# Kernel tuning notes

Hardware: AMD Instinct MI355X
Metric: run time of the kernel (lower is better)

Reference implementation:

```python
import jax, jax.numpy as jnp
import numpy as np


def setup_inputs() -> dict:
    key = jax.random.key(0)
    k1, k2 = jax.random.split(key)
    B, N, D = 32, 8192, 64
    x = jax.random.normal(k1, (B, N, D), dtype=jnp.float32)
    y = jax.random.normal(k2, (B, D, N), dtype=jnp.float32)
    return {"x": x, "y": y}


def reference(x, y):
    # Original: full cdist [B,N,N], mean over batch, take diagonal.
    # Only matched pairs (i,i) survive, so compute them directly —
    # mathematically identical output and gradients.
    y_t = jnp.transpose(y, (0, 2, 1))          # [B, N, D]
    diff = x - y_t                             # [B, N, D]
    pair_dist = jnp.sqrt(jnp.sum(diff * diff, axis=-1))  # [B, N]
    dist_diag = jnp.mean(pair_dist, axis=0)    # [N] == diag(mean_b cdist)
    dist_diag = dist_diag.at[1:3].multiply(1.5)
    loss = jnp.mean(dist_diag)
    return loss
```

## Files before the change

kernel.cpp:

```cpp
#include <hip/hip_runtime.h>


constexpr int B = 32;
constexpr int N = 8192;
constexpr int D = 64;

__global__ __launch_bounds__(256) void euclid_loss_kernel(
    const float* __restrict__ x,
    const float* __restrict__ y,
    float* __restrict__ out)
{
    const int tid = threadIdx.x;
    const int n   = blockIdx.x * 256 + tid;
    const int b   = blockIdx.y;

    const float* xrow = x + ((size_t)b * N + n) * D;
    const float* ycol = y + (size_t)b * D * N + n;

    float acc = 0.0f;
#pragma unroll
    for (int d = 0; d < D; d += 4) {
        const float4 xv = *reinterpret_cast<const float4*>(xrow + d);
        const float y0 = ycol[(size_t)(d + 0) * N];
        const float y1 = ycol[(size_t)(d + 1) * N];
        const float y2 = ycol[(size_t)(d + 2) * N];
        const float y3 = ycol[(size_t)(d + 3) * N];
        const float d0 = xv.x - y0;
        const float d1 = xv.y - y1;
        const float d2 = xv.z - y2;
        const float d3 = xv.w - y3;
        acc += d0 * d0 + d1 * d1 + d2 * d2 + d3 * d3;
    }

    const float w = (n == 1 || n == 2) ? 1.5f : 1.0f;
    float v = w * sqrtf(acc);

#pragma unroll
    for (int off = 32; off > 0; off >>= 1) v += __shfl_down(v, off, 64);

    __shared__ float wsum[4];
    if ((tid & 63) == 0) wsum[tid >> 6] = v;
    __syncthreads();

    if (tid == 0) {
        const float s = (wsum[0] + wsum[1] + wsum[2] + wsum[3]) *
                        (1.0f / (float)(B * N));
        atomicAdd(out, s);
    }
}

extern "C" void kernel_launch(void* const* d_in, const int* in_sizes, int n_in,
                              void* d_out, int out_size, void* d_ws, size_t ws_size,
                              hipStream_t stream) {
    const float* x = (const float*)d_in[0];
    const float* y = (const float*)d_in[1];
    float* out = (float*)d_out;

    hipMemsetAsync(out, 0, sizeof(float), stream);

    dim3 grid(N / 256, B);
    euclid_loss_kernel<<<grid, 256, 0, stream>>>(x, y, out);
}
```

Before: 150.7 us.

## Split each pair's reduction across four threads to improve coalescing and parallelism

Each matched pair is now handled by four threads, each covering sixteen of the feature dimensions, with a shuffle-based reduction combining the partials. All loads are issued up front into registers. The grid grows fourfold, aiming for better x coalescing and more memory-level parallelism. In exchange, y loads are split into smaller contiguous segments and extra shuffles are needed.

```diff
diff --git a/kernel.cpp b/kernel.cpp
--- a/kernel.cpp
+++ b/kernel.cpp
@@ -4,39 +4,53 @@
 constexpr int B = 32;
 constexpr int N = 8192;
 constexpr int D = 64;
+constexpr int TPP = 4;
+constexpr int DC  = D / TPP;
+constexpr int PAIRS_PER_BLOCK = 256 / TPP;
 
 __global__ __launch_bounds__(256) void euclid_loss_kernel(
     const float* __restrict__ x,
     const float* __restrict__ y,
     float* __restrict__ out)
 {
-    const int tid = threadIdx.x;
-    const int n   = blockIdx.x * 256 + tid;
-    const int b   = blockIdx.y;
+    const int tid   = threadIdx.x;
+    const int pair  = tid >> 2;
+    const int chunk = tid & 3;
+    const int n     = blockIdx.x * PAIRS_PER_BLOCK + pair;
+    const int b     = blockIdx.y;
 
-    const float* xrow = x + ((size_t)b * N + n) * D;
-    const float* ycol = y + (size_t)b * D * N + n;
+    const float* xp = x + ((size_t)b * N + n) * D + chunk * DC;
+    const float* yp = y + (size_t)b * D * N + (size_t)(chunk * DC) * N + n;
+
+    float4 xv[4];
+#pragma unroll
+    for (int j = 0; j < 4; ++j)
+        xv[j] = *reinterpret_cast<const float4*>(xp + 4 * j);
+
+    float yv[DC];
+#pragma unroll
+    for (int d = 0; d < DC; ++d)
+        yv[d] = yp[(size_t)d * N];
 
     float acc = 0.0f;
 #pragma unroll
-    for (int d = 0; d < D; d += 4) {
-        const float4 xv = *reinterpret_cast<const float4*>(xrow + d);
-        const float y0 = ycol[(size_t)(d + 0) * N];
-        const float y1 = ycol[(size_t)(d + 1) * N];
-        const float y2 = ycol[(size_t)(d + 2) * N];
-        const float y3 = ycol[(size_t)(d + 3) * N];
-        const float d0 = xv.x - y0;
-        const float d1 = xv.y - y1;
-        const float d2 = xv.z - y2;
-        const float d3 = xv.w - y3;
+    for (int j = 0; j < 4; ++j) {
+        const float d0 = xv[j].x - yv[4 * j + 0];
+        const float d1 = xv[j].y - yv[4 * j + 1];
+        const float d2 = xv[j].z - yv[4 * j + 2];
+        const float d3 = xv[j].w - yv[4 * j + 3];
         acc += d0 * d0 + d1 * d1 + d2 * d2 + d3 * d3;
     }
 
+    acc += __shfl_xor(acc, 1, 64);
+    acc += __shfl_xor(acc, 2, 64);
+
     const float w = (n == 1 || n == 2) ? 1.5f : 1.0f;
-    float v = w * sqrtf(acc);
+    float v = (chunk == 0) ? w * __builtin_sqrtf(acc) : 0.0f;
 
 #pragma unroll
-    for (int off = 32; off > 0; off >>= 1) v += __shfl_down(v, off, 64);
+    for (int off = 4; off < 64; off <<= 1)
+        v += __shfl_xor(v, off, 64);
 
     __shared__ float wsum[4];
     if ((tid & 63) == 0) wsum[tid >> 6] = v;
@@ -58,6 +72,6 @@
 
     hipMemsetAsync(out, 0, sizeof(float), stream);
 
-    dim3 grid(N / 256, B);
+    dim3 grid(N / PAIRS_PER_BLOCK, B);
     euclid_loss_kernel<<<grid, 256, 0, stream>>>(x, y, out);
 }
```

After: 166.7 us. 10.6% more time.
